# Optimization experiments

Hardware: AMD Instinct MI355X
Metric: run time of the kernel (lower is better)

## Reference

```python
import jax, jax.numpy as jnp
import numpy as np


def _ste_sign(x):
    # Binarize to {-1, +1} (sign with sign(0)=+1), straight-through estimator:
    # forward value is sign(x), gradient passes through identity (matches the
    # torch .data-swap trick where autograd sees the fp parameter).
    s = jnp.where(x >= 0, 1.0, -1.0).astype(x.dtype)
    return x + jax.lax.stop_gradient(s - x)


def setup_inputs() -> dict:
    key = jax.random.key(0)
    k1, k2, k3 = jax.random.split(key, 3)
    N, IN, OUT = 8192, 4096, 4096
    x = jax.random.normal(k1, (N, IN), dtype=jnp.float32)
    fp_weight = jax.random.normal(k2, (OUT, IN), dtype=jnp.float32) * 0.02
    bound = 1.0 / np.sqrt(IN)
    fp_bias = jax.random.uniform(k3, (OUT,), dtype=jnp.float32, minval=-bound, maxval=bound)
    return {"x": x, "fp_weight": fp_weight, "fp_bias": fp_bias}


def reference(x, fp_weight, fp_bias):
    # BinarizedLinear forward (training / use_bnn_origin_eval path):
    #   input  -> binarize_tensor (sign quantization to +-1)
    #   weight -> binarize_tensor (sign quantization to +-1)
    #   output = F.linear(bin_input, bin_weight) + bias
    bx = _ste_sign(x)                      # [N, IN]
    bw = _ste_sign(fp_weight)              # [OUT, IN]
    out = jnp.einsum('ni,oi->no', bx, bw)  # [N, OUT]
    out = out + fp_bias[None, :]
    return out
```

## Files before the change

kernel.cpp:

```cpp
#include <hip/hip_runtime.h>
#include <stdint.h>

#define NROW 8192
#define KDIM 4096
#define NOUT 4096

typedef __attribute__((ext_vector_type(4))) int i32x4;

__global__ __launch_bounds__(256)
void bin_i8_fused(const float* __restrict__ x, const float* __restrict__ w,
                  uint32_t* __restrict__ xq, uint32_t* __restrict__ wq,
                  int n4x, int n4tot) {
    int i = blockIdx.x * blockDim.x + threadIdx.x;
    const int stride = gridDim.x * blockDim.x;
    for (; i < n4tot; i += stride) {
        const float4* src;
        uint32_t* dst;
        int j;
        if (i < n4x) { src = (const float4*)x; dst = xq; j = i; }
        else         { src = (const float4*)w; dst = wq; j = i - n4x; }
        float4 v = src[j];
        uint32_t b0 = (v.x < 0.0f) ? 0xFFu : 0x01u;
        uint32_t b1 = (v.y < 0.0f) ? 0xFFu : 0x01u;
        uint32_t b2 = (v.z < 0.0f) ? 0xFFu : 0x01u;
        uint32_t b3 = (v.w < 0.0f) ? 0xFFu : 0x01u;
        dst[j] = b0 | (b1 << 8) | (b2 << 16) | (b3 << 24);
    }
}

#define BM 256
#define BN 256
#define BKB 128
#define NT (KDIM / BKB)

__device__ __forceinline__ void gload_lds16(const void* g, void* l) {
    __builtin_amdgcn_global_load_lds(
        (const __attribute__((address_space(1))) uint32_t*)g,
        (__attribute__((address_space(3))) uint32_t*)l, 16, 0, 0);
}

__global__ __launch_bounds__(512, 2)
void i8_mfma_gemm(const uint8_t* __restrict__ xq, const uint8_t* __restrict__ wq,
                  const float* __restrict__ bias, float* __restrict__ out) {
    __shared__ __align__(16) uint8_t As[2][2][256][64];
    __shared__ __align__(16) uint8_t Bs[2][2][256][64];

    const int tid  = threadIdx.x;
    const int wid  = tid >> 6;
    const int lane = tid & 63;
    const int wr   = wid >> 2;
    const int wc   = wid & 3;
    const int lr   = lane & 15;
    const int g    = lane >> 4;
    const int row0 = blockIdx.y * BM;
    const int col0 = blockIdx.x * BN;

    const int c0 = wid * 64 + lane;
    const int c1 = 512 + c0;
    const int s0 = (((c0 & 3) ^ ((c0 >> 3) & 3))) * 16;
    const int s1 = (((c1 & 3) ^ ((c1 >> 3) & 3))) * 16;
    const int r0 = c0 >> 2;
    const int r1 = c1 >> 2;

    const uint8_t* gA0 = xq + (size_t)(row0 + r0) * KDIM + s0;
    const uint8_t* gA1 = xq + (size_t)(row0 + r1) * KDIM + s1;
    const uint8_t* gB0 = wq + (size_t)(col0 + r0) * KDIM + s0;
    const uint8_t* gB1 = wq + (size_t)(col0 + r1) * KDIM + s1;

    const int sread = (g ^ ((lr >> 1) & 3)) * 16;
    const int ra = wr * 128 + lr;
    const int cb = wc * 64 + lr;

#define STAGE_A(sd, kh, ko) do {                                  \
        uint8_t* _l = &As[sd][kh][0][0];                          \
        gload_lds16(gA0 + (ko) + (kh) * 64, _l + c0 * 16);        \
        gload_lds16(gA1 + (ko) + (kh) * 64, _l + c1 * 16);        \
    } while (0)
#define STAGE_B(sd, kh, ko) do {                                  \
        uint8_t* _l = &Bs[sd][kh][0][0];                          \
        gload_lds16(gB0 + (ko) + (kh) * 64, _l + c0 * 16);        \
        gload_lds16(gB1 + (ko) + (kh) * 64, _l + c1 * 16);        \
    } while (0)

    i32x4 acc[8][4];
#pragma unroll
    for (int m = 0; m < 8; ++m)
#pragma unroll
        for (int n = 0; n < 4; ++n) acc[m][n] = (i32x4){0, 0, 0, 0};

    STAGE_A(0, 0, 0);
    STAGE_B(0, 0, 0);
    STAGE_A(0, 1, 0);
    STAGE_B(0, 1, 0);
    asm volatile("s_waitcnt vmcnt(4)" ::: "memory");
    __builtin_amdgcn_s_barrier();

#pragma unroll 1
    for (int t = 0; t < NT; ++t) {
        const int d  = t & 1;
        const int sd = d ^ 1;
        const int ko = (t + 1 < NT ? t + 1 : t) * BKB;

        i32x4 a0[4], a1[4], b0[4], b1[4];

#pragma unroll
        for (int m = 0; m < 4; ++m)
            a0[m] = *(const i32x4*)&As[d][0][ra + m * 16][sread];
#pragma unroll
        for (int n = 0; n < 4; ++n)
            b0[n] = *(const i32x4*)&Bs[d][0][cb + n * 16][sread];
        STAGE_A(sd, 0, ko);
        __builtin_amdgcn_s_barrier();
        __builtin_amdgcn_s_setprio(1);
#pragma unroll
        for (int m = 0; m < 4; ++m)
#pragma unroll
            for (int n = 0; n < 4; ++n)
                acc[m][n] = __builtin_amdgcn_mfma_i32_16x16x64_i8(
                    a0[m], b0[n], acc[m][n], 0, 0, 0);
        __builtin_amdgcn_s_setprio(0);
        __builtin_amdgcn_s_barrier();

#pragma unroll
        for (int m = 0; m < 4; ++m)
            a1[m] = *(const i32x4*)&As[d][0][ra + 64 + m * 16][sread];
        STAGE_B(sd, 0, ko);
        asm volatile("s_waitcnt vmcnt(4)" ::: "memory");
        __builtin_amdgcn_s_barrier();
        __builtin_amdgcn_s_setprio(1);
#pragma unroll
        for (int m = 0; m < 4; ++m)
#pragma unroll
            for (int n = 0; n < 4; ++n)
                acc[4 + m][n] = __builtin_amdgcn_mfma_i32_16x16x64_i8(
                    a1[m], b0[n], acc[4 + m][n], 0, 0, 0);
        __builtin_amdgcn_s_setprio(0);
        __builtin_amdgcn_s_barrier();

#pragma unroll
        for (int m = 0; m < 4; ++m)
            a0[m] = *(const i32x4*)&As[d][1][ra + m * 16][sread];
#pragma unroll
        for (int n = 0; n < 4; ++n)
            b1[n] = *(const i32x4*)&Bs[d][1][cb + n * 16][sread];
        STAGE_A(sd, 1, ko);
        __builtin_amdgcn_s_barrier();
        __builtin_amdgcn_s_setprio(1);
#pragma unroll
        for (int m = 0; m < 4; ++m)
#pragma unroll
            for (int n = 0; n < 4; ++n)
                acc[m][n] = __builtin_amdgcn_mfma_i32_16x16x64_i8(
                    a0[m], b1[n], acc[m][n], 0, 0, 0);
        __builtin_amdgcn_s_setprio(0);
        __builtin_amdgcn_s_barrier();

#pragma unroll
        for (int m = 0; m < 4; ++m)
            a1[m] = *(const i32x4*)&As[d][1][ra + 64 + m * 16][sread];
        STAGE_B(sd, 1, ko);
        asm volatile("s_waitcnt vmcnt(4)" ::: "memory");
        __builtin_amdgcn_s_barrier();
        __builtin_amdgcn_s_setprio(1);
#pragma unroll
        for (int m = 0; m < 4; ++m)
#pragma unroll
            for (int n = 0; n < 4; ++n)
                acc[4 + m][n] = __builtin_amdgcn_mfma_i32_16x16x64_i8(
                    a1[m], b1[n], acc[4 + m][n], 0, 0, 0);
        __builtin_amdgcn_s_setprio(0);
        __builtin_amdgcn_s_barrier();
    }
#undef STAGE_A
#undef STAGE_B

#pragma unroll
    for (int n = 0; n < 4; ++n) {
        const int col = col0 + wc * 64 + n * 16 + lr;
        const float bv = bias[col];
#pragma unroll
        for (int m = 0; m < 8; ++m) {
            const int rb = row0 + wr * 128 + m * 16 + g * 4;
#pragma unroll
            for (int r = 0; r < 4; ++r)
                out[(size_t)(rb + r) * NOUT + col] = (float)acc[m][n][r] + bv;
        }
    }
}

extern "C" void kernel_launch(void* const* d_in, const int* in_sizes, int n_in,
                              void* d_out, int out_size, void* d_ws, size_t ws_size,
                              hipStream_t stream) {
    const float* x = (const float*)d_in[0];
    const float* w = (const float*)d_in[1];
    const float* b = (const float*)d_in[2];
    float* out = (float*)d_out;

    uint8_t* xq = (uint8_t*)d_ws;
    uint8_t* wq = xq + (size_t)NROW * KDIM;
    (void)ws_size;

    const int n4x = NROW * KDIM / 4;
    const int n4t = n4x + NOUT * KDIM / 4;
    bin_i8_fused<<<3072, 256, 0, stream>>>(x, w, (uint32_t*)xq, (uint32_t*)wq,
                                           n4x, n4t);

    dim3 grid(NOUT / BN, NROW / BM);
    i8_mfma_gemm<<<grid, 512, 0, stream>>>(xq, wq, b, out);
}
```

Before: 422.7 us.

## Software-pipeline LDS fragment reads one phase ahead of MFMA blocks

Restructures the main GEMM loop so that the LDS register fragments for the next MFMA phase are read before the current phase's MFMAs issue. The first fragments are prefetched before the loop, and the next tile's low-A and B0 fragments are loaded at the end of each iteration. The aim is to hide LDS read latency behind matrix-core work rather than stalling at the start of each phase. This adds live vector registers (extra fragment arrays) that could pressure occupancy at 2 blocks/CU, and depends on barrier placement to keep the reads of the just-staged buffer correct.

```diff
diff --git a/kernel.cpp b/kernel.cpp
--- a/kernel.cpp
+++ b/kernel.cpp
@@ -82,11 +82,38 @@
         gload_lds16(gB1 + (ko) + (kh) * 64, _l + c1 * 16);        \
     } while (0)
 
+#define RD_ALO(dst, dd, kh) do {                                       \
+        _Pragma("unroll")                                              \
+        for (int _m = 0; _m < 4; ++_m)                                 \
+            dst[_m] = *(const i32x4*)&As[dd][kh][ra + _m * 16][sread]; \
+    } while (0)
+#define RD_AHI(dst, dd, kh) do {                                       \
+        _Pragma("unroll")                                              \
+        for (int _m = 0; _m < 4; ++_m)                                 \
+            dst[_m] = *(const i32x4*)&As[dd][kh][ra + 64 + _m * 16][sread]; \
+    } while (0)
+#define RD_B(dst, dd, kh) do {                                         \
+        _Pragma("unroll")                                              \
+        for (int _n = 0; _n < 4; ++_n)                                 \
+            dst[_n] = *(const i32x4*)&Bs[dd][kh][cb + _n * 16][sread]; \
+    } while (0)
+#define MFMA_BLK(mb, af, bf) do {                                      \
+        _Pragma("unroll")                                              \
+        for (int _m = 0; _m < 4; ++_m)                                 \
+            _Pragma("unroll")                                          \
+            for (int _n = 0; _n < 4; ++_n)                             \
+                acc[(mb) + _m][_n] = __builtin_amdgcn_mfma_i32_16x16x64_i8( \
+                    af[_m], bf[_n], acc[(mb) + _m][_n], 0, 0, 0);      \
+    } while (0)
+#define FENCE() asm volatile("" ::: "memory")
+
     i32x4 acc[8][4];
 #pragma unroll
     for (int m = 0; m < 8; ++m)
 #pragma unroll
         for (int n = 0; n < 4; ++n) acc[m][n] = (i32x4){0, 0, 0, 0};
+
+    i32x4 aL[4], aH[4], aL2[4], aH2[4], b0[4], b1[4];
 
     STAGE_A(0, 0, 0);
     STAGE_B(0, 0, 0);
@@ -94,6 +121,9 @@
     STAGE_B(0, 1, 0);
     asm volatile("s_waitcnt vmcnt(4)" ::: "memory");
     __builtin_amdgcn_s_barrier();
+    FENCE();
+    RD_ALO(aL, 0, 0);
+    RD_B(b0, 0, 0);
 
 #pragma unroll 1
     for (int t = 0; t < NT; ++t) {
@@ -101,73 +131,41 @@
         const int sd = d ^ 1;
         const int ko = (t + 1 < NT ? t + 1 : t) * BKB;
 
-        i32x4 a0[4], a1[4], b0[4], b1[4];
-
-#pragma unroll
-        for (int m = 0; m < 4; ++m)
-            a0[m] = *(const i32x4*)&As[d][0][ra + m * 16][sread];
-#pragma unroll
-        for (int n = 0; n < 4; ++n)
-            b0[n] = *(const i32x4*)&Bs[d][0][cb + n * 16][sread];
         STAGE_A(sd, 0, ko);
         __builtin_amdgcn_s_barrier();
-        __builtin_amdgcn_s_setprio(1);
-#pragma unroll
-        for (int m = 0; m < 4; ++m)
-#pragma unroll
-            for (int n = 0; n < 4; ++n)
-                acc[m][n] = __builtin_amdgcn_mfma_i32_16x16x64_i8(
-                    a0[m], b0[n], acc[m][n], 0, 0, 0);
-        __builtin_amdgcn_s_setprio(0);
-        __builtin_amdgcn_s_barrier();
-
-#pragma unroll
-        for (int m = 0; m < 4; ++m)
-            a1[m] = *(const i32x4*)&As[d][0][ra + 64 + m * 16][sread];
+        RD_AHI(aH, d, 0);
+        __builtin_amdgcn_s_setprio(1);
+        MFMA_BLK(0, aL, b0);
+        __builtin_amdgcn_s_setprio(0);
+        __builtin_amdgcn_s_barrier();
+
         STAGE_B(sd, 0, ko);
         asm volatile("s_waitcnt vmcnt(4)" ::: "memory");
         __builtin_amdgcn_s_barrier();
-        __builtin_amdgcn_s_setprio(1);
-#pragma unroll
-        for (int m = 0; m < 4; ++m)
-#pragma unroll
-            for (int n = 0; n < 4; ++n)
-                acc[4 + m][n] = __builtin_amdgcn_mfma_i32_16x16x64_i8(
-                    a1[m], b0[n], acc[4 + m][n], 0, 0, 0);
-        __builtin_amdgcn_s_setprio(0);
-        __builtin_amdgcn_s_barrier();
-
-#pragma unroll
-        for (int m = 0; m < 4; ++m)
-            a0[m] = *(const i32x4*)&As[d][1][ra + m * 16][sread];
-#pragma unroll
-        for (int n = 0; n < 4; ++n)
-            b1[n] = *(const i32x4*)&Bs[d][1][cb + n * 16][sread];
+        FENCE();
+        RD_ALO(aL2, d, 1);
+        RD_B(b1, d, 1);
+        __builtin_amdgcn_s_setprio(1);
+        MFMA_BLK(4, aH, b0);
+        __builtin_amdgcn_s_setprio(0);
+        __builtin_amdgcn_s_barrier();
+
         STAGE_A(sd, 1, ko);
         __builtin_amdgcn_s_barrier();
-        __builtin_amdgcn_s_setprio(1);
-#pragma unroll
-        for (int m = 0; m < 4; ++m)
-#pragma unroll
-            for (int n = 0; n < 4; ++n)
-                acc[m][n] = __builtin_amdgcn_mfma_i32_16x16x64_i8(
-                    a0[m], b1[n], acc[m][n], 0, 0, 0);
-        __builtin_amdgcn_s_setprio(0);
-        __builtin_amdgcn_s_barrier();
-
-#pragma unroll
-        for (int m = 0; m < 4; ++m)
-            a1[m] = *(const i32x4*)&As[d][1][ra + 64 + m * 16][sread];
+        RD_AHI(aH2, d, 1);
+        __builtin_amdgcn_s_setprio(1);
+        MFMA_BLK(0, aL2, b1);
+        __builtin_amdgcn_s_setprio(0);
+        __builtin_amdgcn_s_barrier();
+
         STAGE_B(sd, 1, ko);
         asm volatile("s_waitcnt vmcnt(4)" ::: "memory");
         __builtin_amdgcn_s_barrier();
-        __builtin_amdgcn_s_setprio(1);
-#pragma unroll
-        for (int m = 0; m < 4; ++m)
-#pragma unroll
-            for (int n = 0; n < 4; ++n)
-                acc[4 + m][n] = __builtin_amdgcn_mfma_i32_16x16x64_i8(
-                    a1[m], b1[n], acc[4 + m][n], 0, 0, 0);
+        FENCE();
+        RD_ALO(aL, sd, 0);
+        RD_B(b0, sd, 0);
+        __builtin_amdgcn_s_setprio(1);
+        MFMA_BLK(4, aH2, b1);
         __builtin_amdgcn_s_setprio(0);
         __builtin_amdgcn_s_barrier();
     }
```

Result: slower. 438.0 us (+3.6%).
